# Optimization experiments

Hardware: AMD Instinct MI355X
Metric: run time of the kernel (lower is better)

## Reference

```python
import jax, jax.numpy as jnp
import numpy as np

B, S, HID = 2, 2048, 2304
H, KVH, D = 8, 4, 256          # query heads, kv heads, head_dim
N_REP = H // KVH
SCALE = 256.0 ** -0.5          # query_pre_attn_scalar ** -0.5
SOFTCAP = 50.0
ROPE_THETA = 10000.0
NEG = -1e9


def setup_inputs() -> dict:
    key = jax.random.key(0)
    k1, k2, k3, k4, k5 = jax.random.split(key, 5)
    hidden_states = jax.random.normal(k1, (B, S, HID), dtype=jnp.float32)
    # RoPE cos/sin tables, shape [B, S, D]
    inv_freq = 1.0 / (ROPE_THETA ** (jnp.arange(0, D, 2, dtype=jnp.float32) / D))
    pos = jnp.arange(S, dtype=jnp.float32)
    freqs = pos[:, None] * inv_freq[None, :]            # [S, D/2]
    emb = jnp.concatenate([freqs, freqs], axis=-1)      # [S, D]
    cos = jnp.broadcast_to(jnp.cos(emb)[None], (B, S, D))
    sin = jnp.broadcast_to(jnp.sin(emb)[None], (B, S, D))
    # additive causal mask [B, 1, S, S] (sliding_window=4096 > S, so pure causal)
    idx = jnp.arange(S)
    causal = idx[None, :] <= idx[:, None]
    attention_mask = jnp.broadcast_to(
        jnp.where(causal, 0.0, NEG).astype(jnp.float32)[None, None], (B, 1, S, S))
    # projection weights (lecun-normal-ish scale), no bias (attention_bias=False)
    Wq = jax.random.normal(k2, (HID, H * D), dtype=jnp.float32) / np.sqrt(HID)
    Wk = jax.random.normal(k3, (HID, KVH * D), dtype=jnp.float32) / np.sqrt(HID)
    Wv = jax.random.normal(k4, (HID, KVH * D), dtype=jnp.float32) / np.sqrt(HID)
    Wo = jax.random.normal(k5, (H * D, HID), dtype=jnp.float32) / np.sqrt(H * D)
    return {"hidden_states": hidden_states, "cos": cos, "sin": sin,
            "attention_mask": attention_mask,
            "Wq": Wq, "Wk": Wk, "Wv": Wv, "Wo": Wo}


def _rotate_half(x):
    half = x.shape[-1] // 2
    return jnp.concatenate([-x[..., half:], x[..., :half]], axis=-1)


def reference(hidden_states, cos, sin, attention_mask, Wq, Wk, Wv, Wo):
    b, s, _ = hidden_states.shape
    q = (hidden_states @ Wq).reshape(b, s, H, D).transpose(0, 2, 1, 3)    # [B,H,S,D]
    k = (hidden_states @ Wk).reshape(b, s, KVH, D).transpose(0, 2, 1, 3)  # [B,KVH,S,D]
    v = (hidden_states @ Wv).reshape(b, s, KVH, D).transpose(0, 2, 1, 3)
    c = cos[:, None]  # [B,1,S,D] broadcast over heads (unsqueeze_dim=1)
    sn = sin[:, None]
    q = q * c + _rotate_half(q) * sn
    k = k * c + _rotate_half(k) * sn
    # GQA: repeat kv heads (interleave, matching repeat_kv tile+reshape)
    k = jnp.repeat(k, N_REP, axis=1)
    v = jnp.repeat(v, N_REP, axis=1)
    w = jnp.einsum('bhqd,bhkd->bhqk', q, k) * SCALE
    w = jnp.tanh(w / SOFTCAP) * SOFTCAP                  # logit softcapping
    w = w + attention_mask[:, :, :, :s]
    w = jax.nn.softmax(w.astype(jnp.float32), axis=-1).astype(q.dtype)
    out = jnp.einsum('bhqk,bhkd->bhqd', w, v)
    out = out.transpose(0, 2, 1, 3).reshape(b, s, H * D)
    return out @ Wo
```

## Files before the change

### kernel.cpp

```cpp
#include <hip/hip_runtime.h>

typedef unsigned short u16;
typedef __attribute__((ext_vector_type(8))) short short8;
typedef __attribute__((ext_vector_type(4))) float f32x4;
typedef __attribute__((ext_vector_type(4))) unsigned short us4;

constexpr int B_ = 2;
constexpr int H_ = 8;
constexpr int KVH_ = 4;
constexpr int S_ = 2048;
constexpr int D_ = 256;
constexpr int HID_ = 2304;
constexpr int QKVN_ = 4096;
constexpr int AON_ = 2048;

__device__ __forceinline__ float b2f(u16 u) {
  union { float f; unsigned int i; } x; x.i = ((unsigned int)u) << 16; return x.f;
}
__device__ __forceinline__ u16 f2b(float f) {
  unsigned int x = __float_as_uint(f);
  unsigned int r = (x + 0x7fffu + ((x >> 16) & 1u)) >> 16;
  return (u16)r;
}
__device__ __forceinline__ float exp2_raw(float x) {
  float r;
  asm("v_exp_f32 %0, %1" : "=v"(r) : "v"(x));
  return r;
}
__device__ __forceinline__ unsigned int cvt_pk_bf16(float lo, float hi) {
  unsigned int r;
  asm("v_cvt_pk_bf16_f32 %0, %1, %2" : "=v"(r) : "v"(lo), "v"(hi));
  return r;
}

__global__ void prep_kernel(const float* __restrict__ hidden,
                            const float* __restrict__ s0, const float* __restrict__ s1,
                            const float* __restrict__ s2, const float* __restrict__ s3,
                            u16* __restrict__ hsOut,
                            u16* __restrict__ d0, u16* __restrict__ d1,
                            u16* __restrict__ d2, u16* __restrict__ d3) {
  __shared__ float tile[64][65];
  int bx = blockIdx.x;
  int t = threadIdx.x;
  if (bx < 9216) {
    size_t i = ((size_t)bx * 256 + t) * 4;
    float4 v = *(const float4*)(hidden + i);
    unsigned int lo = (unsigned int)f2b(v.x) | ((unsigned int)f2b(v.y) << 16);
    unsigned int hi = (unsigned int)f2b(v.z) | ((unsigned int)f2b(v.w) << 16);
    uint2 o; o.x = lo; o.y = hi;
    *(uint2*)(hsOut + i) = o;
    return;
  }
  int tt = bx - 9216;
  const float* src; u16* dst; int R, C, cx, cy;
  if (tt < 1152)              { src = s0; dst = d0; R = 2304; C = 2048; cx = tt & 31; cy = tt >> 5; }
  else if ((tt -= 1152) < 576){ src = s1; dst = d1; R = 2304; C = 1024; cx = tt & 15; cy = tt >> 4; }
  else if ((tt -= 576) < 576) { src = s2; dst = d2; R = 2304; C = 1024; cx = tt & 15; cy = tt >> 4; }
  else { tt -= 576;             src = s3; dst = d3; R = 2048; C = 2304; cx = tt % 36; cy = tt / 36; }
  int r0 = cy * 64, c0 = cx * 64;
#pragma unroll
  for (int i = 0; i < 16; ++i) {
    int e = i * 256 + t;
    int r = e >> 6, c = e & 63;
    tile[r][c] = src[(size_t)(r0 + r) * C + (c0 + c)];
  }
  __syncthreads();
#pragma unroll
  for (int i = 0; i < 8; ++i) {
    int e = i * 256 + t;
    int orow = e >> 5;
    int ocol = (e & 31) * 2;
    unsigned int w = (unsigned int)f2b(tile[ocol][orow]) |
                     ((unsigned int)f2b(tile[ocol + 1][orow]) << 16);
    *(unsigned int*)(&dst[(size_t)(c0 + orow) * R + (r0 + ocol)]) = w;
  }
}

template <int OUTF32>
__global__ __launch_bounds__(512, 2) void gemm_bt8(
    const u16* __restrict__ A, const u16* __restrict__ B, void* __restrict__ Cp,
    int M, int N, int K) {
  __shared__ u16 lds[2][2][2][8192];
  const int tid = threadIdx.x;
  const int lane = tid & 63;
  const int wave = tid >> 6;
  const int wm = wave >> 2, wn = wave & 3;
  const int quad = lane >> 4, l16 = lane & 15;
  const int m0 = blockIdx.y * 256, n0 = blockIdx.x * 256;
  const int nt = K >> 6;

  const int sub = tid >> 6;
  const int rr = (tid >> 2) & 15;
  const int cc = ((tid & 3) * 8) ^ ((rr & 8) ? 16 : 0);
  const int r_rel = (sub >> 1) * 16 + rr;
  const int ccol = (sub & 1) * 32 + cc;
  const u16* Asrc = A + (size_t)(m0 + r_rel) * K + ccol;
  const u16* Bsrc = B + (size_t)(n0 + r_rel) * K + ccol;
  const int ldsc = tid * 8;

  const int fr_off = l16 * 64 + (((quad * 8) ^ ((l16 & 8) ? 16 : 0)) << 1);

#define GL8(src, dst)                                                                  \
  __builtin_amdgcn_global_load_lds((const __attribute__((address_space(1))) void*)(src), \
                                   (__attribute__((address_space(3))) void*)(dst), 16, 0, 0)
#define STAGE_A(bf, kt, qp) {                                                          \
    const u16* _s = Asrc + (size_t)(kt) * 64;                                          \
    GL8(_s + (size_t)((qp) * 64) * K,       &lds[bf][0][0][(qp) * 4096 + ldsc]);       \
    GL8(_s + (size_t)(128 + (qp) * 64) * K, &lds[bf][0][1][(qp) * 4096 + ldsc]); }
#define STAGE_B(bf, kt, hf) {                                                          \
    const u16* _s = Bsrc + (size_t)(kt) * 64;                                          \
    GL8(_s + (size_t)((hf) * 128) * K,      &lds[bf][1][hf][ldsc]);                    \
    GL8(_s + (size_t)((hf) * 128 + 64) * K, &lds[bf][1][hf][4096 + ldsc]); }
#define LDA(bf, mi, kk) \
  (*(const short8*)((const char*)&lds[bf][0][wm][0] + (mi) * 2048 + (kk) * 1024 + fr_off))
#define LDB(bf, ni, kk) \
  (*(const short8*)((const char*)&lds[bf][1][wn >> 1][0] + ((wn & 1) * 4 + (ni)) * 2048 + (kk) * 1024 + fr_off))

  f32x4 acc[8][4] = {};
  short8 bfr[4][2], af[2][2];

  STAGE_B(0, 0, 0); STAGE_B(0, 0, 1); STAGE_A(0, 0, 0); STAGE_A(0, 0, 1);
  STAGE_B(1, 1, 0); STAGE_B(1, 1, 1); STAGE_A(1, 1, 0);
  asm volatile("s_waitcnt vmcnt(6)" ::: "memory");
  __builtin_amdgcn_s_barrier();

#define PHASE(q, STG, VMW)                                                             \
    _Pragma("unroll") for (int i = 0; i < 2; ++i)                                      \
      _Pragma("unroll") for (int kk = 0; kk < 2; ++kk) af[i][kk] = LDA(c, 2 * (q) + i, kk); \
    STG; VMW;                                                                          \
    __builtin_amdgcn_s_barrier();                                                      \
    asm volatile("s_waitcnt lgkmcnt(0)" ::: "memory");                                 \
    __builtin_amdgcn_sched_barrier(0);                                                 \
    __builtin_amdgcn_s_setprio(1);                                                     \
    _Pragma("unroll") for (int i = 0; i < 2; ++i)                                      \
      _Pragma("unroll") for (int ni = 0; ni < 4; ++ni)                                 \
        _Pragma("unroll") for (int kk = 0; kk < 2; ++kk)                               \
          acc[2 * (q) + i][ni] = __builtin_amdgcn_mfma_f32_16x16x32_bf16(              \
              af[i][kk], bfr[ni][kk], acc[2 * (q) + i][ni], 0, 0, 0);                  \
    __builtin_amdgcn_s_setprio(0);                                                     \
    __builtin_amdgcn_s_barrier();

  for (int T = 0; T < nt; ++T) {
    const int c = T & 1;
#pragma unroll
    for (int ni = 0; ni < 4; ++ni)
#pragma unroll
      for (int kk = 0; kk < 2; ++kk) bfr[ni][kk] = LDB(c, ni, kk);
    PHASE(0, if (T + 1 < nt) STAGE_A(c ^ 1, T + 1, 1), )
    PHASE(1, if (T + 2 < nt) STAGE_B(c, T + 2, 0), )
    PHASE(2, if (T + 2 < nt) STAGE_B(c, T + 2, 1), )
    PHASE(3, if (T + 2 < nt) STAGE_A(c, T + 2, 0),
          if (T + 2 >= nt) { asm volatile("s_waitcnt vmcnt(0)" ::: "memory"); }
          else             { asm volatile("s_waitcnt vmcnt(6)" ::: "memory"); })
  }
#undef PHASE
#undef LDA
#undef LDB
#undef STAGE_A
#undef STAGE_B
#undef GL8

#pragma unroll
  for (int mi = 0; mi < 8; ++mi) {
#pragma unroll
    for (int ni = 0; ni < 4; ++ni) {
#pragma unroll
      for (int r = 0; r < 4; ++r) {
        int row = m0 + wm * 128 + mi * 16 + quad * 4 + r;
        int col = n0 + wn * 64 + ni * 16 + l16;
        if (OUTF32)
          ((float*)Cp)[(size_t)row * N + col] = acc[mi][ni][r];
        else
          ((u16*)Cp)[(size_t)row * N + col] = f2b(acc[mi][ni][r]);
      }
    }
  }
}

template <int OUTF32>
__global__ __launch_bounds__(256, 2) void gemm_bt(
    const u16* __restrict__ A, const u16* __restrict__ B, void* __restrict__ Cp,
    int M, int N, int K) {
  __shared__ u16 As[128 * 32];
  __shared__ u16 Bs[128 * 32];
  int m0 = blockIdx.y * 128, n0 = blockIdx.x * 128;
  int tid = threadIdx.x;
  int lane = tid & 63, wave = tid >> 6;
  int wy = wave >> 1, wx = wave & 1;
  int quad = lane >> 4, l16 = lane & 15;
  f32x4 acc[4][4] = {};
  for (int k0 = 0; k0 < K; k0 += 32) {
#pragma unroll
    for (int i = 0; i < 2; ++i) {
      int chunk = i * 256 + tid;
      int row = chunk >> 2, col = (chunk & 3) << 3;
      __builtin_amdgcn_global_load_lds(
          (const __attribute__((address_space(1))) void*)(A + (size_t)(m0 + row) * K + k0 + col),
          (__attribute__((address_space(3))) void*)(As + chunk * 8), 16, 0, 0);
    }
#pragma unroll
    for (int i = 0; i < 2; ++i) {
      int chunk = i * 256 + tid;
      int row = chunk >> 2, col = (chunk & 3) << 3;
      __builtin_amdgcn_global_load_lds(
          (const __attribute__((address_space(1))) void*)(B + (size_t)(n0 + row) * K + k0 + col),
          (__attribute__((address_space(3))) void*)(Bs + chunk * 8), 16, 0, 0);
    }
    __syncthreads();
    short8 af[4], bf[4];
#pragma unroll
    for (int mi = 0; mi < 4; ++mi)
      af[mi] = *(const short8*)(As + (wy * 64 + mi * 16 + l16) * 32 + quad * 8);
#pragma unroll
    for (int ni = 0; ni < 4; ++ni)
      bf[ni] = *(const short8*)(Bs + (wx * 64 + ni * 16 + l16) * 32 + quad * 8);
#pragma unroll
    for (int mi = 0; mi < 4; ++mi)
#pragma unroll
      for (int ni = 0; ni < 4; ++ni)
        acc[mi][ni] = __builtin_amdgcn_mfma_f32_16x16x32_bf16(af[mi], bf[ni], acc[mi][ni], 0, 0, 0);
    __syncthreads();
  }
#pragma unroll
  for (int mi = 0; mi < 4; ++mi) {
#pragma unroll
    for (int ni = 0; ni < 4; ++ni) {
#pragma unroll
      for (int r = 0; r < 4; ++r) {
        int row = m0 + wy * 64 + mi * 16 + quad * 4 + r;
        int col = n0 + wx * 64 + ni * 16 + l16;
        if (OUTF32)
          ((float*)Cp)[(size_t)row * N + col] = acc[mi][ni][r];
        else
          ((u16*)Cp)[(size_t)row * N + col] = f2b(acc[mi][ni][r]);
      }
    }
  }
}

__global__ void rope_tv_kernel(const u16* __restrict__ qkv, const float* __restrict__ cs,
                               const float* __restrict__ sn, u16* __restrict__ Qr,
                               u16* __restrict__ Kr, u16* __restrict__ Vt) {
  __shared__ u16 tile[64][72];
  int bx = blockIdx.x;
  int t = threadIdx.x;
  if (bx < 512) {
    int row = bx * 8 + (t >> 5);
    int d0 = (t & 31) * 4;
    int b = row >> 11, s = row & 2047;
    const u16* qrow = qkv + (size_t)row * QKVN_;
    float4 c4 = *(const float4*)(cs + (size_t)row * D_ + d0);
    float4 s4 = *(const float4*)(sn + (size_t)row * D_ + d0);
    float c[4] = {c4.x, c4.y, c4.z, c4.w};
    float sv[4] = {s4.x, s4.y, s4.z, s4.w};
#pragma unroll
    for (int h = 0; h < H_ + KVH_; ++h) {
      const u16* src = qrow + (h < H_ ? h * D_ : 2048 + (h - H_) * D_);
      us4 lo = *(const us4*)(src + d0);
      us4 hi = *(const us4*)(src + 128 + d0);
      us4 olo, ohi;
#pragma unroll
      for (int j = 0; j < 4; ++j) {
        float xl = b2f(lo[j]), xh = b2f(hi[j]);
        olo[j] = f2b(xl * c[j] - xh * sv[j]);
        ohi[j] = f2b(xh * c[j] + xl * sv[j]);
      }
      u16* dst = (h < H_)
          ? Qr + ((size_t)(b * H_ + h) * S_ + s) * D_
          : Kr + ((size_t)(b * KVH_ + (h - H_)) * S_ + s) * D_;
      *(us4*)(dst + d0) = olo;
      *(us4*)(dst + 128 + d0) = ohi;
    }
    return;
  }
  int tt = bx - 512;
  int g = tt >> 7;
  int rem = tt & 127;
  int s0 = (rem >> 2) * 64;
  int d0 = (rem & 3) * 64;
  int b = g >> 2, kvh = g & 3;
#pragma unroll
  for (int i = 0; i < 8; ++i) {
    int e = i * 256 + t;
    int r = e >> 5, c = (e & 31) * 2;
    unsigned int v = *(const unsigned int*)(&qkv[(size_t)(b * S_ + s0 + r) * QKVN_ +
                                                 3072 + kvh * D_ + d0 + c]);
    tile[r][c] = (u16)v;
    tile[r][c + 1] = (u16)(v >> 16);
  }
  __syncthreads();
#pragma unroll
  for (int i = 0; i < 8; ++i) {
    int e = i * 256 + t;
    int orow = e >> 5, ocol = (e & 31) * 2;
    unsigned int w = (unsigned int)tile[ocol][orow] |
                     ((unsigned int)tile[ocol + 1][orow] << 16);
    *(unsigned int*)(&Vt[((size_t)g * D_ + d0 + orow) * S_ + s0 + ocol]) = w;
  }
}

__global__ __launch_bounds__(256, 2) void attn_kernel(
    const u16* __restrict__ Qr, const u16* __restrict__ Kr, const u16* __restrict__ Vt,
    float* __restrict__ Op0, float* __restrict__ Op1,
    float* __restrict__ Lp0, float* __restrict__ Lp1) {
  __shared__ u16 Ks[2][32 * 256];
  __shared__ u16 Vs[2][32 * 256];
  int bx = blockIdx.x;
  int h = bx & 7;
  int u = bx >> 4;
  int sp = (bx >> 3) & 1;
  int kvh = h >> 1;
  int tid = threadIdx.x, wave = tid >> 6, lane = tid & 63;
  int quad = lane >> 4, l16 = lane & 15;
  float* Op = sp ? Op1 : Op0;
  float* Lp = sp ? Lp1 : Lp0;
  int ksrc_s[4], ksrc_c[4], vsrc_d[4], vsrc_s[4];
#pragma unroll
  for (int i = 0; i < 4; ++i) {
    int p = i * 256 + tid;
    int sK = p >> 5;
    ksrc_s[i] = sK;
    ksrc_c[i] = (p & 31) ^ ((sK & 3) | (((sK >> 3) & 1) << 2));
    vsrc_d[i] = p >> 2;
    vsrc_s[i] = (p & 3) ^ ((p >> 3) & 3);
  }
  const int kg = l16 >> 2, ka = l16 & 3;
  const int srow0 = 8 * kg + ka;
  const int ksw = ka | ((kg & 1) << 2);

  for (int part = 0; part < 2; ++part) {
    int b = part;
    int qt = (part == 0) ? u : (31 - u);
    int q0 = qt * 64;
    int beg = sp ? (qt + 1) : 0;
    int end = sp ? (2 * qt + 2) : (qt + 1);
    const u16* Qbase = Qr + ((size_t)(b * H_ + h) * S_ + q0 + wave * 16 + l16) * D_;
    short8 qf[8];
#pragma unroll
    for (int kk = 0; kk < 8; ++kk)
      qf[kk] = *(const short8*)(Qbase + kk * 32 + quad * 8);
    const u16* Kbase = Kr + (size_t)(b * KVH_ + kvh) * S_ * D_;
    const u16* Vbase = Vt + (size_t)(b * KVH_ + kvh) * D_ * S_;
    float lp = 0.f;
    f32x4 o_acc[16] = {};
    const int qq = q0 + wave * 16 + l16;

#define STAGE(KT, BUF)                                                                   \
    {                                                                                    \
      int k0s = (KT) * 32;                                                               \
      _Pragma("unroll") for (int i = 0; i < 4; ++i) {                                    \
        int p = i * 256 + tid;                                                           \
        __builtin_amdgcn_global_load_lds(                                                \
            (const __attribute__((address_space(1))) void*)(Kbase +                      \
                (size_t)(k0s + ksrc_s[i]) * D_ + ksrc_c[i] * 8),                         \
            (__attribute__((address_space(3))) void*)(&Ks[BUF][0] + p * 8), 16, 0, 0);   \
      }                                                                                  \
      _Pragma("unroll") for (int i = 0; i < 4; ++i) {                                    \
        int p = i * 256 + tid;                                                           \
        __builtin_amdgcn_global_load_lds(                                                \
            (const __attribute__((address_space(1))) void*)(Vbase +                      \
                (size_t)vsrc_d[i] * S_ + k0s + vsrc_s[i] * 8),                           \
            (__attribute__((address_space(3))) void*)(&Vs[BUF][0] + p * 8), 16, 0, 0);   \
      }                                                                                  \
    }

    STAGE(beg, 0);
    __syncthreads();
    for (int kt = beg; kt < end; ++kt) {
      int k0 = kt * 32;
      int cur = (kt - beg) & 1;
      if (kt + 1 < end) STAGE(kt + 1, cur ^ 1);
      f32x4 sacc[2] = {};
      __builtin_amdgcn_s_setprio(1);
#pragma unroll
      for (int n = 0; n < 2; ++n) {
        const u16* kb = &Ks[cur][0] + (srow0 + 4 * n) * 256;
#pragma unroll
        for (int kk = 0; kk < 8; ++kk) {
          int phys = (kk * 4 + quad) ^ ksw;
          short8 kfr = *(const short8*)(kb + phys * 8);
          sacc[n] = __builtin_amdgcn_mfma_f32_16x16x32_bf16(kfr, qf[kk], sacc[n], 0, 0, 0);
        }
      }
      __builtin_amdgcn_s_setprio(0);
      bool full = (k0 + 31 <= q0 + wave * 16);
#pragma unroll
      for (int n = 0; n < 2; ++n) {
#pragma unroll
        for (int r = 0; r < 4; ++r) {
          float E = exp2_raw(sacc[n][r] * 0.0036067376f);
          float ee = exp2_raw(__frcp_rn(E + 1.0f) * -144.2695041f);
          if (!full) {
            int key = k0 + 8 * quad + 4 * n + r;
            ee = (key <= qq) ? ee : 0.0f;
          }
          lp += ee;
          sacc[n][r] = ee;
        }
      }
      union { short8 s8; unsigned int d[4]; } pu;
      pu.d[0] = cvt_pk_bf16(sacc[0][0], sacc[0][1]);
      pu.d[1] = cvt_pk_bf16(sacc[0][2], sacc[0][3]);
      pu.d[2] = cvt_pk_bf16(sacc[1][0], sacc[1][1]);
      pu.d[3] = cvt_pk_bf16(sacc[1][2], sacc[1][3]);
      short8 pa = pu.s8;
      __builtin_amdgcn_s_setprio(1);
#pragma unroll
      for (int dt = 0; dt < 16; ++dt) {
        int d = dt * 16 + l16;
        int phys = quad ^ ((d >> 1) & 3);
        short8 vb = *(const short8*)(&Vs[cur][0] + d * 32 + phys * 8);
        o_acc[dt] = __builtin_amdgcn_mfma_f32_16x16x32_bf16(pa, vb, o_acc[dt], 0, 0, 0);
      }
      __builtin_amdgcn_s_setprio(0);
      __syncthreads();
    }
#undef STAGE
    lp += __shfl_xor(lp, 16, 64);
    lp += __shfl_xor(lp, 32, 64);
    if (lane < 16)
      Lp[((size_t)(b * H_ + h)) * S_ + q0 + wave * 16 + lane] = lp;
#pragma unroll
    for (int dt = 0; dt < 16; ++dt)
#pragma unroll
      for (int r = 0; r < 4; ++r) {
        int row = b * S_ + q0 + wave * 16 + quad * 4 + r;
        int col = h * D_ + dt * 16 + l16;
        Op[(size_t)row * AON_ + col] = o_acc[dt][r];
      }
  }
}

__global__ void combine_kernel(const float* __restrict__ Op0, const float* __restrict__ Op1,
                               const float* __restrict__ Lp0, const float* __restrict__ Lp1,
                               u16* __restrict__ Ao) {
  size_t idx = (size_t)blockIdx.x * 256 + threadIdx.x;
  size_t row = idx >> 9;
  int c4 = ((int)idx & 511) * 4;
  const float4 a = *(const float4*)(Op0 + row * AON_ + c4);
  const float4 b4 = *(const float4*)(Op1 + row * AON_ + c4);
  int b = (int)(row >> 11), s = (int)row & 2047;
  int h = c4 >> 8;
  size_t li = ((size_t)(b * H_ + h)) * S_ + s;
  float inv = 1.0f / (Lp0[li] + Lp1[li]);
  unsigned int lo = (unsigned int)f2b((a.x + b4.x) * inv) | ((unsigned int)f2b((a.y + b4.y) * inv) << 16);
  unsigned int hi = (unsigned int)f2b((a.z + b4.z) * inv) | ((unsigned int)f2b((a.w + b4.w) * inv) << 16);
  uint2 o; o.x = lo; o.y = hi;
  *(uint2*)(Ao + row * AON_ + c4) = o;
}

extern "C" void kernel_launch(void* const* d_in, const int* in_sizes, int n_in,
                              void* d_out, int out_size, void* d_ws, size_t ws_size,
                              hipStream_t stream) {
  const float* hidden = (const float*)d_in[0];
  const float* cosp = (const float*)d_in[1];
  const float* sinp = (const float*)d_in[2];
  const float* Wq = (const float*)d_in[4];
  const float* Wk = (const float*)d_in[5];
  const float* Wv = (const float*)d_in[6];
  const float* Wo = (const float*)d_in[7];

  u16* hs  = (u16*)d_ws;
  u16* WT  = hs  + (size_t)4096 * HID_;
  u16* WoT = WT  + (size_t)4096 * HID_;
  u16* qkv = WoT + (size_t)HID_ * AON_;
  u16* Qr  = qkv + (size_t)4096 * QKVN_;
  u16* Kr  = Qr  + (size_t)B_ * H_ * S_ * D_;
  u16* Vt  = Kr  + (size_t)B_ * KVH_ * S_ * D_;
  u16* Ao  = Vt  + (size_t)B_ * KVH_ * S_ * D_;
  float* Lp0 = (float*)(Ao + (size_t)4096 * AON_);
  float* Lp1 = Lp0 + (size_t)B_ * H_ * S_;
  float* Op0 = (float*)hs;
  float* Op1 = (float*)qkv;

  prep_kernel<<<12672, 256, 0, stream>>>(
      hidden, Wq, Wk, Wv, Wo, hs,
      WT, WT + (size_t)2048 * HID_, WT + (size_t)3072 * HID_, WoT);
  gemm_bt8<0><<<dim3(16, 16), 512, 0, stream>>>(hs, WT, qkv, 4096, QKVN_, HID_);
  rope_tv_kernel<<<1536, 256, 0, stream>>>(qkv, cosp, sinp, Qr, Kr, Vt);
  attn_kernel<<<dim3(512), 256, 0, stream>>>(Qr, Kr, Vt, Op0, Op1, Lp0, Lp1);
  combine_kernel<<<16384, 256, 0, stream>>>(Op0, Op1, Lp0, Lp1, Ao);
  gemm_bt<1><<<dim3(18, 32), 256, 0, stream>>>(Ao, WoT, d_out, 4096, HID_, 2048);
}
```

Baseline: 390.1 us.

## Fuse split-KV combine into attention via last-arriver atomic flag

Removes the separate combine kernel. Each attention block writes its partial output and sum, then atomically increments a per-tile counter, and the second block to arrive merges both partials and writes the normalized bf16 output. This saves a kernel launch and one pass that re-reads both partial buffers. In exchange it adds a memset, fences and an atomic, and the merging block does extra strided global reads.

```diff
diff --git a/kernel.cpp b/kernel.cpp
--- a/kernel.cpp
+++ b/kernel.cpp
@@ -302,9 +302,11 @@
 __global__ __launch_bounds__(256, 2) void attn_kernel(
     const u16* __restrict__ Qr, const u16* __restrict__ Kr, const u16* __restrict__ Vt,
     float* __restrict__ Op0, float* __restrict__ Op1,
-    float* __restrict__ Lp0, float* __restrict__ Lp1) {
+    float* __restrict__ Lp0, float* __restrict__ Lp1,
+    u16* __restrict__ Ao, int* __restrict__ flags) {
   __shared__ u16 Ks[2][32 * 256];
   __shared__ u16 Vs[2][32 * 256];
+  __shared__ int win;
   int bx = blockIdx.x;
   int h = bx & 7;
   int u = bx >> 4;
@@ -314,6 +316,8 @@
   int quad = lane >> 4, l16 = lane & 15;
   float* Op = sp ? Op1 : Op0;
   float* Lp = sp ? Lp1 : Lp0;
+  const float* Opo = sp ? Op0 : Op1;
+  const float* Lpo = sp ? Lp0 : Lp1;
   int ksrc_s[4], ksrc_c[4], vsrc_d[4], vsrc_s[4];
 #pragma unroll
   for (int i = 0; i < 4; ++i) {
@@ -428,25 +432,30 @@
         int col = h * D_ + dt * 16 + l16;
         Op[(size_t)row * AON_ + col] = o_acc[dt][r];
       }
-  }
-}
-
-__global__ void combine_kernel(const float* __restrict__ Op0, const float* __restrict__ Op1,
-                               const float* __restrict__ Lp0, const float* __restrict__ Lp1,
-                               u16* __restrict__ Ao) {
-  size_t idx = (size_t)blockIdx.x * 256 + threadIdx.x;
-  size_t row = idx >> 9;
-  int c4 = ((int)idx & 511) * 4;
-  const float4 a = *(const float4*)(Op0 + row * AON_ + c4);
-  const float4 b4 = *(const float4*)(Op1 + row * AON_ + c4);
-  int b = (int)(row >> 11), s = (int)row & 2047;
-  int h = c4 >> 8;
-  size_t li = ((size_t)(b * H_ + h)) * S_ + s;
-  float inv = 1.0f / (Lp0[li] + Lp1[li]);
-  unsigned int lo = (unsigned int)f2b((a.x + b4.x) * inv) | ((unsigned int)f2b((a.y + b4.y) * inv) << 16);
-  unsigned int hi = (unsigned int)f2b((a.z + b4.z) * inv) | ((unsigned int)f2b((a.w + b4.w) * inv) << 16);
-  uint2 o; o.x = lo; o.y = hi;
-  *(uint2*)(Ao + row * AON_ + c4) = o;
+    __threadfence();
+    __syncthreads();
+    if (tid == 0) win = atomicAdd(&flags[(b * H_ + h) * 32 + qt], 1);
+    __syncthreads();
+    if (win == 1) {
+      __threadfence();
+      float linv[4];
+#pragma unroll
+      for (int r = 0; r < 4; ++r) {
+        float lown = __shfl(lp, quad * 4 + r, 64);
+        float loth = Lpo[((size_t)(b * H_ + h)) * S_ + q0 + wave * 16 + quad * 4 + r];
+        linv[r] = 1.0f / (lown + loth);
+      }
+#pragma unroll
+      for (int dt = 0; dt < 16; ++dt)
+#pragma unroll
+        for (int r = 0; r < 4; ++r) {
+          size_t row = (size_t)(b * S_ + q0 + wave * 16 + quad * 4 + r);
+          int col = h * D_ + dt * 16 + l16;
+          float v = (o_acc[dt][r] + Opo[row * AON_ + col]) * linv[r];
+          Ao[row * AON_ + col] = f2b(v);
+        }
+    }
+  }
 }
 
 extern "C" void kernel_launch(void* const* d_in, const int* in_sizes, int n_in,
@@ -470,15 +479,16 @@
   u16* Ao  = Vt  + (size_t)B_ * KVH_ * S_ * D_;
   float* Lp0 = (float*)(Ao + (size_t)4096 * AON_);
   float* Lp1 = Lp0 + (size_t)B_ * H_ * S_;
+  int* flags = (int*)(Lp1 + (size_t)B_ * H_ * S_);
   float* Op0 = (float*)hs;
   float* Op1 = (float*)qkv;
 
+  hipMemsetAsync(flags, 0, (size_t)B_ * H_ * 32 * sizeof(int), stream);
   prep_kernel<<<12672, 256, 0, stream>>>(
       hidden, Wq, Wk, Wv, Wo, hs,
       WT, WT + (size_t)2048 * HID_, WT + (size_t)3072 * HID_, WoT);
   gemm_bt8<0><<<dim3(16, 16), 512, 0, stream>>>(hs, WT, qkv, 4096, QKVN_, HID_);
   rope_tv_kernel<<<1536, 256, 0, stream>>>(qkv, cosp, sinp, Qr, Kr, Vt);
-  attn_kernel<<<dim3(512), 256, 0, stream>>>(Qr, Kr, Vt, Op0, Op1, Lp0, Lp1);
-  combine_kernel<<<16384, 256, 0, stream>>>(Op0, Op1, Lp0, Lp1, Ao);
+  attn_kernel<<<dim3(512), 256, 0, stream>>>(Qr, Kr, Vt, Op0, Op1, Lp0, Lp1, Ao, flags);
   gemm_bt<1><<<dim3(18, 32), 256, 0, stream>>>(Ao, WoT, d_out, 4096, HID_, 2048);
 }
```

Measured after the change: 585.1 us. 50.0% more time.

## Fuse RoPE and V transpose into QKV GEMM epilogue via LDS staging

Applied to the files above, without the earlier changes.

The QKV projection GEMM now stages its 256x256 output tile in swizzled LDS. It then applies RoPE directly to produce Qr/Kr, or transposes the tile into Vt, depending on which head column block the workgroup owns. This removes the separate rope_tv kernel launch and the round trip of the intermediate qkv buffer through global memory. Launch bounds drop from 2 to 1 blocks per CU, and the epilogue adds LDS traffic and extra syncs.

```diff
diff --git a/kernel.cpp b/kernel.cpp
--- a/kernel.cpp
+++ b/kernel.cpp
@@ -76,9 +76,10 @@
   }
 }
 
-template <int OUTF32>
-__global__ __launch_bounds__(512, 2) void gemm_bt8(
-    const u16* __restrict__ A, const u16* __restrict__ B, void* __restrict__ Cp,
+__global__ __launch_bounds__(512, 1) void gemm_qkv(
+    const u16* __restrict__ A, const u16* __restrict__ B,
+    const float* __restrict__ cosp, const float* __restrict__ sinp,
+    u16* __restrict__ Qr, u16* __restrict__ Kr, u16* __restrict__ Vt,
     int M, int N, int K) {
   __shared__ u16 lds[2][2][2][8192];
   const int tid = threadIdx.x;
@@ -160,21 +161,67 @@
 #undef STAGE_B
 #undef GL8
 
-#pragma unroll
-  for (int mi = 0; mi < 8; ++mi) {
-#pragma unroll
-    for (int ni = 0; ni < 4; ++ni) {
+  __syncthreads();
+  u16* L = (u16*)&lds[0][0][0][0];
+#define SWZ(row, col) (((row) * 256) + ((col) ^ (((row) & 15) << 3)))
+#pragma unroll
+  for (int mi = 0; mi < 8; ++mi)
+#pragma unroll
+    for (int ni = 0; ni < 4; ++ni)
 #pragma unroll
       for (int r = 0; r < 4; ++r) {
-        int row = m0 + wm * 128 + mi * 16 + quad * 4 + r;
-        int col = n0 + wn * 64 + ni * 16 + l16;
-        if (OUTF32)
-          ((float*)Cp)[(size_t)row * N + col] = acc[mi][ni][r];
-        else
-          ((u16*)Cp)[(size_t)row * N + col] = f2b(acc[mi][ni][r]);
-      }
-    }
-  }
+        int rowl = wm * 128 + mi * 16 + quad * 4 + r;
+        int coll = wn * 64 + ni * 16 + l16;
+        L[SWZ(rowl, coll)] = f2b(acc[mi][ni][r]);
+      }
+  __syncthreads();
+  const int ci = blockIdx.x;
+  const int bb = m0 >> 11;
+  const int s0l = m0 & 2047;
+  if (ci < 12) {
+    int rowl = tid >> 1;
+    int dbase = (tid & 1) << 6;
+    size_t srow = (size_t)(m0 + rowl);
+    const float* cb = cosp + srow * D_ + dbase;
+    const float* sb = sinp + srow * D_ + dbase;
+    u16* dst = (ci < 8)
+        ? Qr + ((size_t)(bb * H_ + ci) * S_ + s0l + rowl) * D_ + dbase
+        : Kr + ((size_t)(bb * KVH_ + (ci - 8)) * S_ + s0l + rowl) * D_ + dbase;
+#pragma unroll
+    for (int j = 0; j < 64; j += 4) {
+      float4 c4 = *(const float4*)(cb + j);
+      float4 s4 = *(const float4*)(sb + j);
+      int d = dbase + j;
+      us4 xl4 = *(const us4*)(L + SWZ(rowl, d));
+      us4 xh4 = *(const us4*)(L + SWZ(rowl, d + 128));
+      float cc2[4] = {c4.x, c4.y, c4.z, c4.w};
+      float ss2[4] = {s4.x, s4.y, s4.z, s4.w};
+      us4 olo, ohi;
+#pragma unroll
+      for (int jj = 0; jj < 4; ++jj) {
+        float xl = b2f(xl4[jj]), xh = b2f(xh4[jj]);
+        olo[jj] = f2b(xl * cc2[jj] - xh * ss2[jj]);
+        ohi[jj] = f2b(xh * cc2[jj] + xl * ss2[jj]);
+      }
+      *(us4*)(dst + j) = olo;
+      *(us4*)(dst + 128 + j) = ohi;
+    }
+  } else {
+    size_t gg = (size_t)(bb * KVH_ + (ci - 12));
+#pragma unroll
+    for (int i = 0; i < 32; ++i) {
+      int d = wave * 32 + i;
+      u16* vdst = Vt + (gg * D_ + d) * S_ + s0l;
+#pragma unroll
+      for (int half = 0; half < 2; ++half) {
+        int s2 = half * 128 + lane * 2;
+        unsigned int w = (unsigned int)L[SWZ(s2, d)] |
+                         ((unsigned int)L[SWZ(s2 + 1, d)] << 16);
+        *(unsigned int*)(vdst + s2) = w;
+      }
+    }
+  }
+#undef SWZ
 }
 
 template <int OUTF32>
@@ -235,67 +282,6 @@
           ((u16*)Cp)[(size_t)row * N + col] = f2b(acc[mi][ni][r]);
       }
     }
-  }
-}
-
-__global__ void rope_tv_kernel(const u16* __restrict__ qkv, const float* __restrict__ cs,
-                               const float* __restrict__ sn, u16* __restrict__ Qr,
-                               u16* __restrict__ Kr, u16* __restrict__ Vt) {
-  __shared__ u16 tile[64][72];
-  int bx = blockIdx.x;
-  int t = threadIdx.x;
-  if (bx < 512) {
-    int row = bx * 8 + (t >> 5);
-    int d0 = (t & 31) * 4;
-    int b = row >> 11, s = row & 2047;
-    const u16* qrow = qkv + (size_t)row * QKVN_;
-    float4 c4 = *(const float4*)(cs + (size_t)row * D_ + d0);
-    float4 s4 = *(const float4*)(sn + (size_t)row * D_ + d0);
-    float c[4] = {c4.x, c4.y, c4.z, c4.w};
-    float sv[4] = {s4.x, s4.y, s4.z, s4.w};
-#pragma unroll
-    for (int h = 0; h < H_ + KVH_; ++h) {
-      const u16* src = qrow + (h < H_ ? h * D_ : 2048 + (h - H_) * D_);
-      us4 lo = *(const us4*)(src + d0);
-      us4 hi = *(const us4*)(src + 128 + d0);
-      us4 olo, ohi;
-#pragma unroll
-      for (int j = 0; j < 4; ++j) {
-        float xl = b2f(lo[j]), xh = b2f(hi[j]);
-        olo[j] = f2b(xl * c[j] - xh * sv[j]);
-        ohi[j] = f2b(xh * c[j] + xl * sv[j]);
-      }
-      u16* dst = (h < H_)
-          ? Qr + ((size_t)(b * H_ + h) * S_ + s) * D_
-          : Kr + ((size_t)(b * KVH_ + (h - H_)) * S_ + s) * D_;
-      *(us4*)(dst + d0) = olo;
-      *(us4*)(dst + 128 + d0) = ohi;
-    }
-    return;
-  }
-  int tt = bx - 512;
-  int g = tt >> 7;
-  int rem = tt & 127;
-  int s0 = (rem >> 2) * 64;
-  int d0 = (rem & 3) * 64;
-  int b = g >> 2, kvh = g & 3;
-#pragma unroll
-  for (int i = 0; i < 8; ++i) {
-    int e = i * 256 + t;
-    int r = e >> 5, c = (e & 31) * 2;
-    unsigned int v = *(const unsigned int*)(&qkv[(size_t)(b * S_ + s0 + r) * QKVN_ +
-                                                 3072 + kvh * D_ + d0 + c]);
-    tile[r][c] = (u16)v;
-    tile[r][c + 1] = (u16)(v >> 16);
-  }
-  __syncthreads();
-#pragma unroll
-  for (int i = 0; i < 8; ++i) {
-    int e = i * 256 + t;
-    int orow = e >> 5, ocol = (e & 31) * 2;
-    unsigned int w = (unsigned int)tile[ocol][orow] |
-                     ((unsigned int)tile[ocol + 1][orow] << 16);
-    *(unsigned int*)(&Vt[((size_t)g * D_ + d0 + orow) * S_ + s0 + ocol]) = w;
   }
 }
 
@@ -476,8 +462,8 @@
   prep_kernel<<<12672, 256, 0, stream>>>(
       hidden, Wq, Wk, Wv, Wo, hs,
       WT, WT + (size_t)2048 * HID_, WT + (size_t)3072 * HID_, WoT);
-  gemm_bt8<0><<<dim3(16, 16), 512, 0, stream>>>(hs, WT, qkv, 4096, QKVN_, HID_);
-  rope_tv_kernel<<<1536, 256, 0, stream>>>(qkv, cosp, sinp, Qr, Kr, Vt);
+  gemm_qkv<<<dim3(16, 16), 512, 0, stream>>>(
+      hs, WT, cosp, sinp, Qr, Kr, Vt, 4096, QKVN_, HID_);
   attn_kernel<<<dim3(512), 256, 0, stream>>>(Qr, Kr, Vt, Op0, Op1, Lp0, Lp1);
   combine_kernel<<<16384, 256, 0, stream>>>(Op0, Op1, Lp0, Lp1, Ao);
   gemm_bt<1><<<dim3(18, 32), 256, 0, stream>>>(Ao, WoT, d_out, 4096, HID_, 2048);
```

After: 399.1 us. +2.3%, slower.
